# Kernel optimization log

Hardware: AMD Instinct MI355X
Metric: run time of the kernel (lower is better)

Reference implementation:

```python
import jax, jax.numpy as jnp
import numpy as np

B, S, D, HEADS = 2, 1024, 1024, 16
DK = D // HEADS           # 64: size of the 'heads' axis after split (namedtensor quirk)
LOW = D // DK             # 16: size of the contracted 'lower' axis
SCALE = float(D)          # Attention(p, scale=d_model) -> divide by d_model
NEG = -1.0e9


def setup_inputs() -> dict:
    key = jax.random.key(0)
    ks = jax.random.split(key, 8)
    query = jax.random.normal(ks[0], (B, S, D), dtype=jnp.float32)
    key_t = jax.random.normal(ks[1], (B, S, D), dtype=jnp.float32)
    value = jax.random.normal(ks[2], (B, S, D), dtype=jnp.float32)
    mask = jax.random.bernoulli(ks[3], 0.25, (B, S, S))  # True -> masked out
    std = 1.0 / np.sqrt(D)
    Wq = jax.random.normal(ks[4], (D, D), dtype=jnp.float32) * std
    Wk = jax.random.normal(ks[5], (D, D), dtype=jnp.float32) * std
    Wv = jax.random.normal(ks[6], (D, D), dtype=jnp.float32) * std
    Wo = jax.random.normal(ks[7], (D, D), dtype=jnp.float32) * std
    return {"query": query, "key": key_t, "value": value, "mask": mask,
            "Wq": Wq, "Wk": Wk, "Wv": Wv, "Wo": Wo}


def reference(query, key, value, mask, Wq, Wk, Wv, Wo):
    # nn.Linear(d_model, d_model, bias=False): y = x @ W.T
    def split(x, W):
        y = jnp.einsum('bsd,ed->bse', x, W)
        return y.reshape(B, -1, DK, LOW)  # hidden -> ('heads'=DK, 'lower'=LOW)

    q = split(query, Wq)   # [B,Sq,H,L] with H=DK, L=LOW
    k = split(key, Wk)     # [B,Sk,H,L]
    v = split(value, Wv)   # [B,Sk,H,L]

    # scores = query.dot('lower', key) / d_model  -> contract the LOW axis
    scores = jnp.einsum('bqhl,bkhl->bhqk', q, k) / SCALE
    scores = jnp.where(mask[:, None, :, :], NEG, scores)  # scores[mask] = -1e9
    p_attn = jax.nn.softmax(scores, axis=-1)  # softmax over keys; dropout=eval

    # value.dot('keys', p_attn) -> [B,H,L,Q]; stack ('heads','lower') -> hidden
    x = jnp.einsum('bkhl,bhqk->bqhl', v, p_attn).reshape(B, -1, D)
    return jnp.einsum('bsd,ed->bse', x, Wo)
```

## Files before the change

### kernel.cpp

```cpp
#include <hip/hip_runtime.h>
#include <hip/hip_bf16.h>


typedef __hip_bfloat16 bf16;
typedef __attribute__((ext_vector_type(8))) short short8;
typedef __attribute__((ext_vector_type(4))) float f32x4;
typedef __attribute__((ext_vector_type(16))) float f32x16;

__device__ __forceinline__ unsigned short f2bf(float f) {
  union { float f; unsigned u; } x; x.f = f;
  unsigned r = x.u + 0x7FFFu + ((x.u >> 16) & 1u);
  return (unsigned short)(r >> 16);
}

__device__ __forceinline__ unsigned cvt_pk_bf16(float lo, float hi) {
  unsigned r;
  asm("v_cvt_pk_bf16_f32 %0, %1, %2" : "=v"(r) : "v"(lo), "v"(hi));
  return r;
}

__device__ __forceinline__ float fast_exp2(float x) {
#if __has_builtin(__builtin_amdgcn_exp2f)
  return __builtin_amdgcn_exp2f(x);
#else
  return __expf(x * 0.6931471805599453f);
#endif
}

__device__ __forceinline__ void gload16(const void* g, void* l) {
#if __has_builtin(__builtin_amdgcn_global_load_lds)
  __builtin_amdgcn_global_load_lds(
      (const __attribute__((address_space(1))) unsigned*)g,
      (__attribute__((address_space(3))) unsigned*)l, 16, 0, 0);
#else
  *(uint4*)l = *(const uint4*)g;
#endif
}

__global__ void convert_all(
    const float* __restrict__ s0, const float* __restrict__ s1, const float* __restrict__ s2,
    const float* __restrict__ s3, const float* __restrict__ s4, const float* __restrict__ s5,
    const float* __restrict__ s6,
    bf16* __restrict__ d0, bf16* __restrict__ d1, bf16* __restrict__ d2,
    bf16* __restrict__ d3, bf16* __restrict__ d4, bf16* __restrict__ d5,
    bf16* __restrict__ d6,
    const unsigned char* __restrict__ mB, const int* __restrict__ mI,
    unsigned* __restrict__ mout) {
  const int z = blockIdx.y;
  if (z == 7) {
    if (blockIdx.x >= 256) return;
    __shared__ int sflag;
    if (threadIdx.x == 0) sflag = 0;
    __syncthreads();
    const int widx = blockIdx.x * 256 + threadIdx.x;
    const int row = widx >> 5, kb = widx & 31;
    uchar4 v[8];
    const uchar4* p = (const uchar4*)(mB + (size_t)row * 1024 + kb * 32);
    unsigned any = 0;
#pragma unroll
    for (int j = 0; j < 8; ++j) { v[j] = p[j]; any |= (unsigned)v[j].y | (unsigned)v[j].z | (unsigned)v[j].w; }
    if (__ballot(any != 0)) { if ((threadIdx.x & 63) == 0) atomicOr(&sflag, 1); }
    __syncthreads();
    unsigned bits = 0;
    if (sflag) {
#pragma unroll
      for (int j = 0; j < 8; ++j) {
        bits |= ((unsigned)(v[j].x != 0) << (4 * j)) | ((unsigned)(v[j].y != 0) << (4 * j + 1))
              | ((unsigned)(v[j].z != 0) << (4 * j + 2)) | ((unsigned)(v[j].w != 0) << (4 * j + 3));
      }
    } else {
      const int4* q = (const int4*)(mI + (size_t)row * 1024 + kb * 32);
#pragma unroll
      for (int j = 0; j < 8; ++j) {
        int4 u = q[j];
        bits |= ((unsigned)(u.x != 0) << (4 * j)) | ((unsigned)(u.y != 0) << (4 * j + 1))
              | ((unsigned)(u.z != 0) << (4 * j + 2)) | ((unsigned)(u.w != 0) << (4 * j + 3));
      }
    }
    const int bq = row >> 10, qb = (row & 1023) >> 5, qr = row & 31;
    mout[((((bq * 32 + qb) * 8 + (kb >> 2)) * 32 + qr) << 2) + (kb & 3)] = bits;
    return;
  }
  const float* s; bf16* d; int n8; float sc = 1.0f;
  if      (z == 0) { s = s0; d = d0; n8 = 262144; }
  else if (z == 1) { s = s1; d = d1; n8 = 262144; }
  else if (z == 2) { s = s2; d = d2; n8 = 262144; }
  else if (z == 3) { s = s3; d = d3; n8 = 131072; sc = 0.0014088818758681283f; }
  else if (z == 4) { s = s4; d = d4; n8 = 131072; }
  else if (z == 5) { s = s5; d = d5; n8 = 131072; }
  else             { s = s6; d = d6; n8 = 131072; }
  const int i = blockIdx.x * 256 + threadIdx.x;
  if (i >= n8) return;
  const f32x4* p = (const f32x4*)s + (size_t)i * 2;
  f32x4 a = p[0], b = p[1];
  uint4 o;
  o.x = cvt_pk_bf16(a[0] * sc, a[1] * sc); o.y = cvt_pk_bf16(a[2] * sc, a[3] * sc);
  o.z = cvt_pk_bf16(b[0] * sc, b[1] * sc); o.w = cvt_pk_bf16(b[2] * sc, b[3] * sc);
  ((uint4*)d)[i] = o;
}

#define PSTR 36

__global__ __launch_bounds__(256) void gemm_qkv(
    const bf16* __restrict__ A0, const bf16* __restrict__ A1, const bf16* __restrict__ A2,
    const bf16* __restrict__ W0, const bf16* __restrict__ W1, const bf16* __restrict__ W2,
    bf16* __restrict__ C0, bf16* __restrict__ C1, bf16* __restrict__ C2) {
  __shared__ __align__(16) bf16 smem[12288];
  bf16* As = smem;
  bf16* Bs = smem + 8192;
  const int z = blockIdx.z;
  const bf16* __restrict__ A = (z == 0) ? A0 : (z == 1) ? A1 : A2;
  const bf16* __restrict__ W = (z == 0) ? W0 : (z == 1) ? W1 : W2;
  bf16* __restrict__ C = (z == 0) ? C0 : (z == 1) ? C1 : C2;
  const int tid = threadIdx.x, lane = tid & 63, w = tid >> 6;
  const int wr = (w >> 1) * 64, wc = (w & 1) * 32;
  const int row0 = blockIdx.y * 128, col0 = blockIdx.x * 64;
  const int l15 = lane & 15, kg = lane >> 4;
  const int l7 = l15 & 7;

  const bf16* ga[4]; const bf16* gb[2];
  bf16* la[4]; bf16* lb[2];
#pragma unroll
  for (int r = 0; r < 4; ++r) {
    const int idx = r * 256 + tid, row = idx >> 3, g = idx & 7;
    ga[r] = A + (size_t)(row0 + row) * 1024 + (g ^ (row & 7)) * 8;
    la[r] = As + idx * 8;
  }
#pragma unroll
  for (int r = 0; r < 2; ++r) {
    const int idx = r * 256 + tid, row = idx >> 3, g = idx & 7;
    gb[r] = W + (size_t)(col0 + row) * 1024 + (g ^ (row & 7)) * 8;
    lb[r] = Bs + idx * 8;
  }

  f32x4 acc[4][2];
#pragma unroll
  for (int m = 0; m < 4; ++m)
#pragma unroll
    for (int n = 0; n < 2; ++n)
#pragma unroll
      for (int j = 0; j < 4; ++j) acc[m][n][j] = 0.f;

  for (int t = 0; t < 16; ++t) {
    const int k0 = t * 64;
#pragma unroll
    for (int r = 0; r < 4; ++r) gload16(ga[r] + k0, la[r]);
#pragma unroll
    for (int r = 0; r < 2; ++r) gload16(gb[r] + k0, lb[r]);
    __syncthreads();
    short8 af[4][2], bfr[2][2];
#pragma unroll
    for (int m = 0; m < 4; ++m)
#pragma unroll
      for (int ks = 0; ks < 2; ++ks)
        af[m][ks] = *(const short8*)(&As[(wr + m * 16 + l15) * 64 + ((ks * 4 + kg) ^ l7) * 8]);
#pragma unroll
    for (int n = 0; n < 2; ++n)
#pragma unroll
      for (int ks = 0; ks < 2; ++ks)
        bfr[n][ks] = *(const short8*)(&Bs[(wc + n * 16 + l15) * 64 + ((ks * 4 + kg) ^ l7) * 8]);
#pragma unroll
    for (int ks = 0; ks < 2; ++ks)
#pragma unroll
      for (int m = 0; m < 4; ++m)
#pragma unroll
        for (int n = 0; n < 2; ++n)
          acc[m][n] = __builtin_amdgcn_mfma_f32_16x16x32_bf16(af[m][ks], bfr[n][ks], acc[m][n], 0, 0, 0);
    __syncthreads();
  }

  const int bb = row0 >> 10, srel0 = row0 & 1023;
  if (z == 2) {
    bf16* T = smem;
#pragma unroll
    for (int m = 0; m < 4; ++m)
#pragma unroll
      for (int n = 0; n < 2; ++n) {
        const int e = wc + n * 16 + l15;
        const int rb = wr + m * 16 + kg * 4;
        uint2 u;
        u.x = cvt_pk_bf16(acc[m][n][0], acc[m][n][1]);
        u.y = cvt_pk_bf16(acc[m][n][2], acc[m][n][3]);
        *(uint2*)(T + e * 136 + rb) = u;
      }
    __syncthreads();
#pragma unroll
    for (int i = 0; i < 4; ++i) {
      const int idx = i * 256 + tid;
      const int tile = idx >> 6, within = idx & 63;
      const int hl = tile >> 2, kbl = tile & 3;
      const int e_sub = within >> 2, kq4 = within & 3;
      uint4 v = *(const uint4*)(T + (hl * 16 + e_sub) * 136 + kbl * 32 + kq4 * 8);
      const int h = (col0 >> 4) + hl;
      const size_t kb = (size_t)((srel0 >> 5) + kbl);
      *(uint4*)((unsigned short*)C + (((size_t)(bb * 64 + h) * 32 + kb) * 512 + e_sub * 32 + kq4 * 8)) = v;
    }
  } else if (z == 1) {
#pragma unroll
    for (int m = 0; m < 4; ++m)
#pragma unroll
      for (int n = 0; n < 2; ++n) {
        const int ecol = wc + n * 16 + l15;
        const int h = (col0 >> 4) + (ecol >> 4), d = ecol & 15;
#pragma unroll
        for (int j = 0; j < 4; ++j) {
          const int s = srel0 + wr + m * 16 + kg * 4 + j;
          ((unsigned short*)C)[((size_t)(bb * 64 + h) * 32 + (s >> 5)) * 512 + (s & 31) * 16 + d] =
              f2bf(acc[m][n][j]);
        }
      }
  } else {
#pragma unroll
    for (int m = 0; m < 4; ++m)
#pragma unroll
      for (int n = 0; n < 2; ++n) {
        const int col = col0 + wc + n * 16 + l15;
#pragma unroll
        for (int j = 0; j < 4; ++j) {
          const int row = row0 + wr + m * 16 + kg * 4 + j;
          ((unsigned short*)C)[(size_t)row * 1024 + col] = f2bf(acc[m][n][j]);
        }
      }
  }
}

__global__ __launch_bounds__(256) void gemm_out(
    const bf16* __restrict__ A, const bf16* __restrict__ W, float* __restrict__ C) {
  __shared__ __align__(16) bf16 smem[12288];
  bf16* As = smem;
  bf16* Bs = smem + 8192;
  const int tid = threadIdx.x, lane = tid & 63, w = tid >> 6;
  const int wr = (w >> 1) * 64, wc = (w & 1) * 32;
  const int row0 = blockIdx.y * 128, col0 = blockIdx.x * 64;
  const int l15 = lane & 15, kg = lane >> 4;
  const int l7 = l15 & 7;

  const bf16* ga[4]; const bf16* gb[2];
  bf16* la[4]; bf16* lb[2];
#pragma unroll
  for (int r = 0; r < 4; ++r) {
    const int idx = r * 256 + tid, row = idx >> 3, g = idx & 7;
    ga[r] = A + (size_t)(row0 + row) * 1024 + (g ^ (row & 7)) * 8;
    la[r] = As + idx * 8;
  }
#pragma unroll
  for (int r = 0; r < 2; ++r) {
    const int idx = r * 256 + tid, row = idx >> 3, g = idx & 7;
    gb[r] = W + (size_t)(col0 + row) * 1024 + (g ^ (row & 7)) * 8;
    lb[r] = Bs + idx * 8;
  }

  f32x4 acc[4][2];
#pragma unroll
  for (int m = 0; m < 4; ++m)
#pragma unroll
    for (int n = 0; n < 2; ++n)
#pragma unroll
      for (int j = 0; j < 4; ++j) acc[m][n][j] = 0.f;

  for (int t = 0; t < 16; ++t) {
    const int k0 = t * 64;
#pragma unroll
    for (int r = 0; r < 4; ++r) gload16(ga[r] + k0, la[r]);
#pragma unroll
    for (int r = 0; r < 2; ++r) gload16(gb[r] + k0, lb[r]);
    __syncthreads();
    short8 af[4][2], bfr[2][2];
#pragma unroll
    for (int m = 0; m < 4; ++m)
#pragma unroll
      for (int ks = 0; ks < 2; ++ks)
        af[m][ks] = *(const short8*)(&As[(wr + m * 16 + l15) * 64 + ((ks * 4 + kg) ^ l7) * 8]);
#pragma unroll
    for (int n = 0; n < 2; ++n)
#pragma unroll
      for (int ks = 0; ks < 2; ++ks)
        bfr[n][ks] = *(const short8*)(&Bs[(wc + n * 16 + l15) * 64 + ((ks * 4 + kg) ^ l7) * 8]);
#pragma unroll
    for (int ks = 0; ks < 2; ++ks)
#pragma unroll
      for (int m = 0; m < 4; ++m)
#pragma unroll
        for (int n = 0; n < 2; ++n)
          acc[m][n] = __builtin_amdgcn_mfma_f32_16x16x32_bf16(af[m][ks], bfr[n][ks], acc[m][n], 0, 0, 0);
    __syncthreads();
  }

#pragma unroll
  for (int m = 0; m < 4; ++m)
#pragma unroll
    for (int n = 0; n < 2; ++n) {
      const int col = col0 + wc + n * 16 + l15;
#pragma unroll
      for (int j = 0; j < 4; ++j) {
        const int row = row0 + wr + m * 16 + kg * 4 + j;
        C[(size_t)row * 1024 + col] = acc[m][n][j];
      }
    }
}

__global__ __launch_bounds__(256) void attn_kernel(
    const bf16* __restrict__ Qp, const bf16* __restrict__ KT, const bf16* __restrict__ VT,
    const unsigned* __restrict__ mw, bf16* __restrict__ XO) {
  __shared__ bf16 Pl[4][2][32 * PSTR];
  const int tid = threadIdx.x, lane = tid & 63, w = tid >> 6;
  const int hi = lane >> 5, l31 = lane & 31, l15 = lane & 15, kg = lane >> 4;
  const int id = blockIdx.x;
  const int xcd = id & 7, grp = (id >> 3) & 15, qt = id >> 7;
  const int g = xcd * 16 + grp;
  const int b = g >> 6, h = g & 63;
  const int qg = w >> 1, kh = w & 1;
  const int q0 = qt * 64 + qg * 32;

  const short8 qf = *(const short8*)(Qp + ((size_t)(b * 1024 + q0 + l31)) * 1024 + h * 16 + hi * 8);
  const bf16* __restrict__ Kb = KT + ((size_t)(b * 64 + h) * 32) * 512;
  const bf16* __restrict__ Vb = VT + ((size_t)(b * 64 + h) * 32) * 512;
  const uint4* __restrict__ Mq =
      (const uint4*)mw + ((size_t)((b * 32 + (q0 >> 5)) * 8 + kh * 4)) * 32 + l31;
  const int sh4 = hi * 4;

  const uint4 mqa = Mq[0], mqb = Mq[32], mqc = Mq[64], mqd = Mq[96];
  const unsigned mm[16] = {mqa.x, mqa.y, mqa.z, mqa.w, mqb.x, mqb.y, mqb.z, mqb.w,
                           mqc.x, mqc.y, mqc.z, mqc.w, mqd.x, mqd.y, mqd.z, mqd.w};

  f32x4 acc0, acc1, sum0, sum1;
#pragma unroll
  for (int j = 0; j < 4; ++j) { acc0[j] = 0.f; acc1[j] = 0.f; sum0[j] = 0.f; sum1[j] = 0.f; }
  f32x16 Z;
#pragma unroll
  for (int i = 0; i < 16; ++i) Z[i] = 0.f;
  short8 ones;
#pragma unroll
  for (int i = 0; i < 8; ++i) ones[i] = (short)0x3F80;

  short8 pa0p, pa1p, vfp;

#pragma unroll
  for (int t = 0; t < 16; ++t) {
    const int kbg = kh * 16 + t;
    const unsigned mword = mm[t] >> sh4;
    const short8 kf = *(const short8*)(Kb + (size_t)kbg * 512 + l31 * 16 + hi * 8);
    f32x16 S = __builtin_amdgcn_mfma_f32_32x32x16_bf16(kf, qf, Z, 0, 0, 0);

    if (t > 0) {
      __builtin_amdgcn_s_setprio(1);
      acc0 = __builtin_amdgcn_mfma_f32_16x16x32_bf16(pa0p, vfp, acc0, 0, 0, 0);
      acc1 = __builtin_amdgcn_mfma_f32_16x16x32_bf16(pa1p, vfp, acc1, 0, 0, 0);
      sum0 = __builtin_amdgcn_mfma_f32_16x16x32_bf16(pa0p, ones, sum0, 0, 0, 0);
      sum1 = __builtin_amdgcn_mfma_f32_16x16x32_bf16(pa1p, ones, sum1, 0, 0, 0);
      __builtin_amdgcn_s_setprio(0);
    }

    bf16* pw = &Pl[w][t & 1][l31 * PSTR];
#pragma unroll
    for (int gg = 0; gg < 4; ++gg) {
      float p0, p1, p2, p3;
      p0 = (mword & (1u << (8 * gg + 0))) ? 0.f : fast_exp2(S[4 * gg + 0]);
      p1 = (mword & (1u << (8 * gg + 1))) ? 0.f : fast_exp2(S[4 * gg + 1]);
      p2 = (mword & (1u << (8 * gg + 2))) ? 0.f : fast_exp2(S[4 * gg + 2]);
      p3 = (mword & (1u << (8 * gg + 3))) ? 0.f : fast_exp2(S[4 * gg + 3]);
      uint2 u;
      u.x = cvt_pk_bf16(p0, p1);
      u.y = cvt_pk_bf16(p2, p3);
      *(uint2*)(pw + 8 * gg + 4 * hi) = u;
    }

    vfp  = *(const short8*)(Vb + (size_t)kbg * 512 + l15 * 32 + kg * 8);
    pa0p = *(const short8*)(&Pl[w][t & 1][l15 * PSTR + kg * 8]);
    pa1p = *(const short8*)(&Pl[w][t & 1][(16 + l15) * PSTR + kg * 8]);
  }

  __builtin_amdgcn_s_setprio(1);
  acc0 = __builtin_amdgcn_mfma_f32_16x16x32_bf16(pa0p, vfp, acc0, 0, 0, 0);
  acc1 = __builtin_amdgcn_mfma_f32_16x16x32_bf16(pa1p, vfp, acc1, 0, 0, 0);
  sum0 = __builtin_amdgcn_mfma_f32_16x16x32_bf16(pa0p, ones, sum0, 0, 0, 0);
  sum1 = __builtin_amdgcn_mfma_f32_16x16x32_bf16(pa1p, ones, sum1, 0, 0, 0);
  __builtin_amdgcn_s_setprio(0);

  float* fl = (float*)&Pl[0][0][0];
  __syncthreads();
  if (kh) {
    float* dst = fl + ((size_t)(qg * 64 + lane)) * 16;
#pragma unroll
    for (int j = 0; j < 4; ++j) {
      dst[j] = acc0[j]; dst[4 + j] = acc1[j]; dst[8 + j] = sum0[j]; dst[12 + j] = sum1[j];
    }
  }
  __syncthreads();
  if (!kh) {
    const float* src = fl + ((size_t)(qg * 64 + lane)) * 16;
#pragma unroll
    for (int j = 0; j < 4; ++j) {
      const float o0 = acc0[j] + src[j],      d0 = sum0[j] + src[8 + j];
      const float o1 = acc1[j] + src[4 + j],  d1 = sum1[j] + src[12 + j];
      const size_t colo = (size_t)h * 16 + l15;
      ((unsigned short*)XO)[((size_t)(b * 1024 + q0 + kg * 4 + j)) * 1024 + colo] = f2bf(o0 / d0);
      ((unsigned short*)XO)[((size_t)(b * 1024 + q0 + 16 + kg * 4 + j)) * 1024 + colo] = f2bf(o1 / d1);
    }
  }
}

extern "C" void kernel_launch(void* const* d_in, const int* in_sizes, int n_in,
                              void* d_out, int out_size, void* d_ws, size_t ws_size,
                              hipStream_t stream) {
  const float* query = (const float*)d_in[0];
  const float* key   = (const float*)d_in[1];
  const float* value = (const float*)d_in[2];
  const void*  mask  = d_in[3];
  const float* Wq = (const float*)d_in[4];
  const float* Wk = (const float*)d_in[5];
  const float* Wv = (const float*)d_in[6];
  const float* Wo = (const float*)d_in[7];
  float* out = (float*)d_out;

  char* ws = (char*)d_ws;
  const size_t MB = 1024 * 1024;
  unsigned* mbits = (unsigned*)(ws + 4096);
  bf16* Qb  = (bf16*)(ws + 4096 + 262144);
  bf16* Kb  = Qb + 2 * MB;
  bf16* Vb  = Kb + 2 * MB;
  bf16* Wqb = Vb + 2 * MB;
  bf16* Wkb = Wqb + MB;
  bf16* Wvb = Wkb + MB;
  bf16* Wob = Wvb + MB;
  bf16* Qp  = Wob + MB;
  bf16* KTl = Qp + 2 * MB;
  bf16* VTl = KTl + 2 * MB;
  bf16* XO  = VTl + 2 * MB;

  convert_all<<<dim3(1024, 8), 256, 0, stream>>>(query, key, value, Wq, Wk, Wv, Wo,
                                                 Qb, Kb, Vb, Wqb, Wkb, Wvb, Wob,
                                                 (const unsigned char*)mask, (const int*)mask,
                                                 mbits);
  gemm_qkv<<<dim3(16, 16, 3), 256, 0, stream>>>(Qb, Kb, Vb, Wqb, Wkb, Wvb, Qp, KTl, VTl);
  attn_kernel<<<dim3(2048), 256, 0, stream>>>(Qp, KTl, VTl, mbits, XO);
  gemm_out<<<dim3(16, 16), 256, 0, stream>>>(XO, Wob, out);
}
```

Before: 87.96 us.

## Keep softmax probabilities in registers via lane shuffles and fold row sums into PV MFMA

The attention kernel stops staging the bf16 probability tile through LDS. It now rebuilds the A operand for the PV product with cross-half lane shuffles, and uses a 32x32x16 MFMA whose upper 16 columns multiply against ones, so the softmax denominator comes out of the same instruction. K fragments and mask words are prefetched one step ahead, and the final division uses a hardware reciprocal. This removes the per-iteration LDS write/read round trip and two of the four MFMAs, at the cost of extra shuffle/select VALU work and half of the PV MFMA columns spent on sums.

```diff
diff --git a/kernel.cpp b/kernel.cpp
--- a/kernel.cpp
+++ b/kernel.cpp
@@ -24,6 +24,14 @@
   return __builtin_amdgcn_exp2f(x);
 #else
   return __expf(x * 0.6931471805599453f);
+#endif
+}
+
+__device__ __forceinline__ float fast_rcp(float x) {
+#if __has_builtin(__builtin_amdgcn_rcpf)
+  return __builtin_amdgcn_rcpf(x);
+#else
+  return 1.0f / x;
 #endif
 }
 
@@ -99,8 +107,6 @@
   ((uint4*)d)[i] = o;
 }
 
-#define PSTR 36
-
 __global__ __launch_bounds__(256) void gemm_qkv(
     const bf16* __restrict__ A0, const bf16* __restrict__ A1, const bf16* __restrict__ A2,
     const bf16* __restrict__ W0, const bf16* __restrict__ W1, const bf16* __restrict__ W2,
@@ -302,9 +308,9 @@
 __global__ __launch_bounds__(256) void attn_kernel(
     const bf16* __restrict__ Qp, const bf16* __restrict__ KT, const bf16* __restrict__ VT,
     const unsigned* __restrict__ mw, bf16* __restrict__ XO) {
-  __shared__ bf16 Pl[4][2][32 * PSTR];
+  __shared__ float Cmb[128 * 17];
   const int tid = threadIdx.x, lane = tid & 63, w = tid >> 6;
-  const int hi = lane >> 5, l31 = lane & 31, l15 = lane & 15, kg = lane >> 4;
+  const int hi = lane >> 5, l31 = lane & 31, l15 = lane & 15;
   const int id = blockIdx.x;
   const int xcd = id & 7, grp = (id >> 3) & 15, qt = id >> 7;
   const int g = xcd * 16 + grp;
@@ -319,83 +325,81 @@
       (const uint4*)mw + ((size_t)((b * 32 + (q0 >> 5)) * 8 + kh * 4)) * 32 + l31;
   const int sh4 = hi * 4;
 
-  const uint4 mqa = Mq[0], mqb = Mq[32], mqc = Mq[64], mqd = Mq[96];
-  const unsigned mm[16] = {mqa.x, mqa.y, mqa.z, mqa.w, mqb.x, mqb.y, mqb.z, mqb.w,
-                           mqc.x, mqc.y, mqc.z, mqc.w, mqd.x, mqd.y, mqd.z, mqd.w};
-
-  f32x4 acc0, acc1, sum0, sum1;
-#pragma unroll
-  for (int j = 0; j < 4; ++j) { acc0[j] = 0.f; acc1[j] = 0.f; sum0[j] = 0.f; sum1[j] = 0.f; }
-  f32x16 Z;
-#pragma unroll
-  for (int i = 0; i < 16; ++i) Z[i] = 0.f;
+  f32x16 acc, Z;
+#pragma unroll
+  for (int i = 0; i < 16; ++i) { acc[i] = 0.f; Z[i] = 0.f; }
   short8 ones;
 #pragma unroll
   for (int i = 0; i < 8; ++i) ones[i] = (short)0x3F80;
 
-  short8 pa0p, pa1p, vfp;
+  short8 kf = *(const short8*)(Kb + (size_t)(kh * 16) * 512 + l31 * 16 + hi * 8);
+  uint4 mq = Mq[0];
 
 #pragma unroll
   for (int t = 0; t < 16; ++t) {
     const int kbg = kh * 16 + t;
-    const unsigned mword = mm[t] >> sh4;
-    const short8 kf = *(const short8*)(Kb + (size_t)kbg * 512 + l31 * 16 + hi * 8);
+    const unsigned mword =
+        (((t & 3) == 0) ? mq.x : ((t & 3) == 1) ? mq.y : ((t & 3) == 2) ? mq.z : mq.w) >> sh4;
+    short8 kfn;
+    if (t < 15) kfn = *(const short8*)(Kb + (size_t)(kbg + 1) * 512 + l31 * 16 + hi * 8);
+    if ((t & 3) == 3 && t < 15) mq = Mq[(t / 4 + 1) * 32];
+    const bf16* vt = Vb + (size_t)kbg * 512 + l15 * 32 + hi * 8;
+    const short8 vraw1 = *(const short8*)(vt);
+    const short8 vraw2 = *(const short8*)(vt + 16);
+
     f32x16 S = __builtin_amdgcn_mfma_f32_32x32x16_bf16(kf, qf, Z, 0, 0, 0);
 
-    if (t > 0) {
-      __builtin_amdgcn_s_setprio(1);
-      acc0 = __builtin_amdgcn_mfma_f32_16x16x32_bf16(pa0p, vfp, acc0, 0, 0, 0);
-      acc1 = __builtin_amdgcn_mfma_f32_16x16x32_bf16(pa1p, vfp, acc1, 0, 0, 0);
-      sum0 = __builtin_amdgcn_mfma_f32_16x16x32_bf16(pa0p, ones, sum0, 0, 0, 0);
-      sum1 = __builtin_amdgcn_mfma_f32_16x16x32_bf16(pa1p, ones, sum1, 0, 0, 0);
-      __builtin_amdgcn_s_setprio(0);
+    unsigned c[8], sw[8];
+#pragma unroll
+    for (int gg = 0; gg < 4; ++gg) {
+      const float p0 = (mword & (1u << (8 * gg + 0))) ? 0.f : fast_exp2(S[4 * gg + 0]);
+      const float p1 = (mword & (1u << (8 * gg + 1))) ? 0.f : fast_exp2(S[4 * gg + 1]);
+      const float p2 = (mword & (1u << (8 * gg + 2))) ? 0.f : fast_exp2(S[4 * gg + 2]);
+      const float p3 = (mword & (1u << (8 * gg + 3))) ? 0.f : fast_exp2(S[4 * gg + 3]);
+      c[2 * gg]     = cvt_pk_bf16(p0, p1);
+      c[2 * gg + 1] = cvt_pk_bf16(p2, p3);
     }
-
-    bf16* pw = &Pl[w][t & 1][l31 * PSTR];
-#pragma unroll
-    for (int gg = 0; gg < 4; ++gg) {
-      float p0, p1, p2, p3;
-      p0 = (mword & (1u << (8 * gg + 0))) ? 0.f : fast_exp2(S[4 * gg + 0]);
-      p1 = (mword & (1u << (8 * gg + 1))) ? 0.f : fast_exp2(S[4 * gg + 1]);
-      p2 = (mword & (1u << (8 * gg + 2))) ? 0.f : fast_exp2(S[4 * gg + 2]);
-      p3 = (mword & (1u << (8 * gg + 3))) ? 0.f : fast_exp2(S[4 * gg + 3]);
-      uint2 u;
-      u.x = cvt_pk_bf16(p0, p1);
-      u.y = cvt_pk_bf16(p2, p3);
-      *(uint2*)(pw + 8 * gg + 4 * hi) = u;
-    }
-
-    vfp  = *(const short8*)(Vb + (size_t)kbg * 512 + l15 * 32 + kg * 8);
-    pa0p = *(const short8*)(&Pl[w][t & 1][l15 * PSTR + kg * 8]);
-    pa1p = *(const short8*)(&Pl[w][t & 1][(16 + l15) * PSTR + kg * 8]);
-  }
-
-  __builtin_amdgcn_s_setprio(1);
-  acc0 = __builtin_amdgcn_mfma_f32_16x16x32_bf16(pa0p, vfp, acc0, 0, 0, 0);
-  acc1 = __builtin_amdgcn_mfma_f32_16x16x32_bf16(pa1p, vfp, acc1, 0, 0, 0);
-  sum0 = __builtin_amdgcn_mfma_f32_16x16x32_bf16(pa0p, ones, sum0, 0, 0, 0);
-  sum1 = __builtin_amdgcn_mfma_f32_16x16x32_bf16(pa1p, ones, sum1, 0, 0, 0);
-  __builtin_amdgcn_s_setprio(0);
-
-  float* fl = (float*)&Pl[0][0][0];
+#pragma unroll
+    for (int i = 0; i < 8; ++i) sw[i] = (unsigned)__shfl_xor((int)c[i], 32, 64);
+
+    uint4 fa1, fa2;
+    fa1.x = hi ? sw[2] : c[0];  fa1.y = hi ? sw[3] : c[1];
+    fa1.z = hi ? c[2]  : sw[0]; fa1.w = hi ? c[3]  : sw[1];
+    fa2.x = hi ? sw[6] : c[4];  fa2.y = hi ? sw[7] : c[5];
+    fa2.z = hi ? c[6]  : sw[4]; fa2.w = hi ? c[7]  : sw[5];
+    short8 A1 = *(const short8*)&fa1;
+    short8 A2 = *(const short8*)&fa2;
+
+    const short8 vb1 = (l31 < 16) ? vraw1 : ones;
+    const short8 vb2 = (l31 < 16) ? vraw2 : ones;
+
+    __builtin_amdgcn_s_setprio(1);
+    acc = __builtin_amdgcn_mfma_f32_32x32x16_bf16(A1, vb1, acc, 0, 0, 0);
+    acc = __builtin_amdgcn_mfma_f32_32x32x16_bf16(A2, vb2, acc, 0, 0, 0);
+    __builtin_amdgcn_s_setprio(0);
+    kf = kfn;
+  }
+
   __syncthreads();
   if (kh) {
-    float* dst = fl + ((size_t)(qg * 64 + lane)) * 16;
-#pragma unroll
-    for (int j = 0; j < 4; ++j) {
-      dst[j] = acc0[j]; dst[4 + j] = acc1[j]; dst[8 + j] = sum0[j]; dst[12 + j] = sum1[j];
-    }
+    float* dst = Cmb + ((size_t)(qg * 64 + lane)) * 17;
+#pragma unroll
+    for (int j = 0; j < 16; ++j) dst[j] = acc[j];
   }
   __syncthreads();
   if (!kh) {
-    const float* src = fl + ((size_t)(qg * 64 + lane)) * 16;
-#pragma unroll
-    for (int j = 0; j < 4; ++j) {
-      const float o0 = acc0[j] + src[j],      d0 = sum0[j] + src[8 + j];
-      const float o1 = acc1[j] + src[4 + j],  d1 = sum1[j] + src[12 + j];
-      const size_t colo = (size_t)h * 16 + l15;
-      ((unsigned short*)XO)[((size_t)(b * 1024 + q0 + kg * 4 + j)) * 1024 + colo] = f2bf(o0 / d0);
-      ((unsigned short*)XO)[((size_t)(b * 1024 + q0 + 16 + kg * 4 + j)) * 1024 + colo] = f2bf(o1 / d1);
+    const float* src = Cmb + ((size_t)(qg * 64 + lane)) * 17;
+    float o[16];
+#pragma unroll
+    for (int j = 0; j < 16; ++j) o[j] = acc[j] + src[j];
+#pragma unroll
+    for (int r = 0; r < 16; ++r) {
+      const float s = __shfl_xor(o[r], 16, 64);
+      if (l31 < 16) {
+        const int q = (r & 3) + 8 * (r >> 2) + 4 * hi;
+        ((unsigned short*)XO)[((size_t)(b * 1024 + q0 + q)) * 1024 + h * 16 + l31] =
+            f2bf(o[r] * fast_rcp(s));
+      }
     }
   }
 }
```

After: 91.78 us. 1.04x slower.
